# Optimization experiments

Measured on AMD Instinct MI355X. Metric: run time of the kernel, lower is better.

## Reference

```python
import jax, jax.numpy as jnp
import numpy as np

B, S, E = 2, 4096, 768
NH, D = 12, 64
W = 256            # one-sided attention window (attention_window=512 // 2)
NEG = jnp.float32(-1e30)  # stands in for -inf at invalid band positions (safe grads)


def setup_inputs() -> dict:
    key = jax.random.key(0)
    ks = jax.random.split(key, 4)
    sc = 0.02
    return {
        'hidden_states': jax.random.normal(ks[0], (B, S, E), jnp.float32),
        'attention_mask': jnp.zeros((B, S), jnp.float32),   # 0 = local attention everywhere
        'is_index_masked': jnp.zeros((B, S), bool),
        'Wq': jax.random.normal(ks[1], (E, E), jnp.float32) * sc,
        'bq': jnp.zeros((E,), jnp.float32),
        'Wk': jax.random.normal(ks[2], (E, E), jnp.float32) * sc,
        'bk': jnp.zeros((E,), jnp.float32),
        'Wv': jax.random.normal(ks[3], (E, E), jnp.float32) * sc,
        'bv': jnp.zeros((E,), jnp.float32),
    }


def _longformer_local(hidden_states, attention_mask, is_index_masked, Wq, bq, Wk, bk, Wv, bv):
    b, s, e = hidden_states.shape
    w = W
    nc = s // w
    # projections (nn.Linear: x @ W.T + b); query pre-scaled by 1/sqrt(head_dim)
    q = (hidden_states @ Wq.T + bq) / jnp.sqrt(jnp.float32(D))
    k = hidden_states @ Wk.T + bk
    v = hidden_states @ Wv.T + bv
    # [B, NH, S, D]
    q = q.reshape(b, s, NH, D).transpose(0, 2, 1, 3)
    k = k.reshape(b, s, NH, D).transpose(0, 2, 1, 3)
    v = v.reshape(b, s, NH, D).transpose(0, 2, 1, 3)

    # pad keys/values by w on each side; chunk into [B,NH,nc,3w,D] windows
    kp = jnp.pad(k, ((0, 0), (0, 0), (w, w), (0, 0)))
    vp = jnp.pad(v, ((0, 0), (0, 0), (w, w), (0, 0)))
    starts = jnp.arange(nc) * w                      # [nc]
    cidx = starts[:, None] + jnp.arange(3 * w)[None, :]  # [nc, 3w] (padded coords)
    kc = kp[:, :, cidx, :]                            # [B,NH,nc,3w,D]
    vc = vp[:, :, cidx, :]                            # [B,NH,nc,3w,D]
    qc = q.reshape(b, NH, nc, w, D)

    # banded scores: query p in chunk attends keys at offsets p..p+2w within the 3w window
    scores = jnp.einsum('bhcpd,bhckd->bhcpk', qc, kc)  # [B,NH,nc,w,3w]
    p = jnp.arange(w)[:, None]
    koff = jnp.arange(2 * w + 1)[None, :]
    band_idx = p + koff                                # [w, 2w+1]
    band = jnp.take_along_axis(scores, band_idx[None, None, None], axis=-1)  # [B,NH,nc,w,2w+1]

    # additive mask from attention_mask (torch: finfo.min where !=0), gathered at key positions
    fmask = jnp.where(attention_mask != 0, jnp.finfo(jnp.float32).min, jnp.float32(0.0))  # [B,S]
    j = starts[:, None, None] + band_idx[None] - w     # global key index [nc,w,2w+1]
    valid = (j >= 0) & (j < s)
    jc = jnp.clip(j, 0, s - 1)
    band = band + fmask[:, jc][:, None]                # [B,1->NH,nc,w,2w+1]
    # _mask_invalid_locations: out-of-sequence band entries -> -inf (NEG)
    band = jnp.where(valid[None, None], band, NEG)

    probs = jax.nn.softmax(band.astype(jnp.float32), axis=-1)
    # zero probs at fully-masked query positions
    im = is_index_masked.reshape(b, 1, nc, w, 1)
    probs = jnp.where(im, jnp.float32(0.0), probs)

    # scatter band back to [B,NH,nc,w,3w] and contract with value chunks
    full = jnp.zeros((b, NH, nc, w, 3 * w), probs.dtype).at[:, :, :, p, band_idx].set(probs)
    out = jnp.einsum('bhcpk,bhckd->bhcpd', full, vc)   # [B,NH,nc,w,D]
    out = out.reshape(b, NH, s, D).transpose(0, 2, 1, 3).reshape(b, s, e)
    return out


def reference(hidden_states, attention_mask, is_index_masked, Wq, bq, Wk, bk, Wv, bv):
    return _longformer_local(hidden_states, attention_mask, is_index_masked,
                             Wq, bq, Wk, bk, Wv, bv)
```

## Files before the change

kernel.cpp:

```cpp
#include <hip/hip_runtime.h>

typedef __bf16 bf16;
typedef __attribute__((ext_vector_type(8))) __bf16 bf16x8;
typedef __attribute__((ext_vector_type(4))) __bf16 bf16x4;
typedef __attribute__((ext_vector_type(4))) float f32x4;

#define MFMA16(a, b, c) __builtin_amdgcn_mfma_f32_16x16x32_bf16((a), (b), (c), 0, 0, 0)

#define S_LEN 4096
#define NHEAD 12
#define EMB   768
#define NEGV  (-1e30f)

__global__ __launch_bounds__(256) void cvt_kernel(const float* __restrict__ x,
                                                  bf16* __restrict__ o, int n8, float scale) {
  int i = blockIdx.x * 256 + threadIdx.x;
  if (i >= n8) return;
  const float4* p = (const float4*)(x + (size_t)i * 8);
  float4 a = p[0], b = p[1];
  bf16x8 v;
  v[0] = (bf16)(a.x * scale); v[1] = (bf16)(a.y * scale);
  v[2] = (bf16)(a.z * scale); v[3] = (bf16)(a.w * scale);
  v[4] = (bf16)(b.x * scale); v[5] = (bf16)(b.y * scale);
  v[6] = (bf16)(b.z * scale); v[7] = (bf16)(b.w * scale);
  *(bf16x8*)(o + (size_t)i * 8) = v;
}

__global__ __launch_bounds__(256) void qkv_gemm(const bf16* __restrict__ Xb, const bf16* __restrict__ Wb,
                                                const float* __restrict__ bq, const float* __restrict__ bk,
                                                const float* __restrict__ bv,
                                                bf16* __restrict__ Qo, bf16* __restrict__ Ko,
                                                bf16* __restrict__ Vt) {
  __shared__ union SM {
    struct { bf16 a[128 * 64]; bf16 b[128 * 64]; } st;
    bf16 c[128 * 130];
  } sm;
  const int tid = threadIdx.x;
  const int l = tid & 63, w = tid >> 6;
  const int ln = l & 15, g = l >> 4;
  const int wm = w >> 1, wn = w & 1;
  const int m0 = blockIdx.x * 128;
  const int n0 = blockIdx.y * 128;

  const f32x4 zero4 = {0.f, 0.f, 0.f, 0.f};
  f32x4 acc[4][4];
#pragma unroll
  for (int i = 0; i < 4; ++i)
#pragma unroll
    for (int j = 0; j < 4; ++j) acc[i][j] = zero4;

  for (int kt = 0; kt < 12; ++kt) {
    const int k0 = kt * 64;
#pragma unroll
    for (int p = 0; p < 4; ++p) {
      int G = p * 256 + tid;
      int row = G >> 3, slot = G & 7;
      int dsl = slot ^ (row & 7);
      bf16x8 va = *(const bf16x8*)(Xb + (size_t)(m0 + row) * 768 + k0 + slot * 8);
      *(bf16x8*)(&sm.st.a[row * 64 + dsl * 8]) = va;
      bf16x8 vb = *(const bf16x8*)(Wb + (size_t)(n0 + row) * 768 + k0 + slot * 8);
      *(bf16x8*)(&sm.st.b[row * 64 + dsl * 8]) = vb;
    }
    __syncthreads();
#pragma unroll
    for (int kc = 0; kc < 2; ++kc) {
      bf16x8 af[4], bfr[4];
#pragma unroll
      for (int i = 0; i < 4; ++i) {
        int ra = wm * 64 + i * 16 + ln;
        af[i] = *(const bf16x8*)(&sm.st.a[ra * 64 + ((kc * 4 + g) ^ (ra & 7)) * 8]);
        int rb = wn * 64 + i * 16 + ln;
        bfr[i] = *(const bf16x8*)(&sm.st.b[rb * 64 + ((kc * 4 + g) ^ (rb & 7)) * 8]);
      }
#pragma unroll
      for (int mi = 0; mi < 4; ++mi)
#pragma unroll
        for (int ni = 0; ni < 4; ++ni)
          acc[mi][ni] = MFMA16(af[mi], bfr[ni], acc[mi][ni]);
    }
    __syncthreads();
  }

  const int which = n0 / 768;
  const int h0 = (n0 % 768) >> 6;
  const int b = m0 >> 12;
  const int h = h0 + wn;
  const float bsc = (which == 0) ? 0.125f : 1.0f;
  const float* bias = (which == 0) ? bq : (which == 1) ? bk : bv;
  float bvv[4];
#pragma unroll
  for (int ni = 0; ni < 4; ++ni) bvv[ni] = bias[h * 64 + ni * 16 + ln] * bsc;

  if (which < 2) {
    bf16* dst = (which == 0) ? Qo : Ko;
    const size_t base = ((size_t)(b * NHEAD + h) * S_LEN + (m0 & 4095)) * 64;
#pragma unroll
    for (int mi = 0; mi < 4; ++mi)
#pragma unroll
      for (int ni = 0; ni < 4; ++ni)
#pragma unroll
        for (int r = 0; r < 4; ++r) {
          int sl = wm * 64 + mi * 16 + g * 4 + r;
          dst[base + (size_t)sl * 64 + ni * 16 + ln] = (bf16)(acc[mi][ni][r] + bvv[ni]);
        }
  } else {
#pragma unroll
    for (int mi = 0; mi < 4; ++mi)
#pragma unroll
      for (int ni = 0; ni < 4; ++ni)
#pragma unroll
        for (int r = 0; r < 4; ++r) {
          int sl = wm * 64 + mi * 16 + g * 4 + r;
          sm.c[sl * 130 + wn * 64 + ni * 16 + ln] = (bf16)(acc[mi][ni][r] + bvv[ni]);
        }
    __syncthreads();
#pragma unroll
    for (int it = 0; it < 4; ++it) {
      int d = it * 32 + (tid >> 3);
      int scp = tid & 7;
      int hh = h0 + (d >> 6);
      bf16x8 o0, o1;
#pragma unroll
      for (int i2 = 0; i2 < 8; ++i2) o0[i2] = sm.c[(scp * 16 + i2) * 130 + d];
#pragma unroll
      for (int i2 = 0; i2 < 8; ++i2) o1[i2] = sm.c[(scp * 16 + 8 + i2) * 130 + d];
      bf16* dp = Vt + ((size_t)(b * NHEAD + hh) * 64 + (d & 63)) * S_LEN + (m0 & 4095) + scp * 16;
      *(bf16x8*)dp = o0;
      *(bf16x8*)(dp + 8) = o1;
    }
  }
}

__global__ __launch_bounds__(256) void attn_kernel(const bf16* __restrict__ Qb, const bf16* __restrict__ Kb,
                                                   const bf16* __restrict__ Vtb,
                                                   const float* __restrict__ amask,
                                                   const unsigned char* __restrict__ imask,
                                                   float* __restrict__ out) {
  __shared__ bf16 Ks[64 * 64];
  __shared__ bf16 Vs[64 * 64];
  __shared__ bf16 Pt[4][16 * 64];
  __shared__ float Ams[64];
  const int tid = threadIdx.x;
  const int l = tid & 63, w = tid >> 6;
  const int ln = l & 15, g = l >> 4;
  const int bh = blockIdx.y, b = bh / NHEAD, h = bh % NHEAD;
  const int q0 = blockIdx.x * 64;
  const int qg = q0 + w * 16 + ln;

  const size_t qoff = ((size_t)bh * S_LEN + qg) * 64;
  const bf16x8 qf0 = *(const bf16x8*)(Qb + qoff + g * 8);
  const bf16x8 qf1 = *(const bf16x8*)(Qb + qoff + 32 + g * 8);

  const f32x4 zero4 = {0.f, 0.f, 0.f, 0.f};
  f32x4 acc[4];
#pragma unroll
  for (int i = 0; i < 4; ++i) acc[i] = zero4;
  float mrun = -1e38f, lrun = 0.f;

  for (int t = 0; t < 9; ++t) {
    const int tj0 = q0 - 256 + t * 64;
    if (tj0 < 0 || tj0 >= S_LEN) continue;
#pragma unroll
    for (int p = 0; p < 2; ++p) {
      int G = p * 256 + tid;
      int row = G >> 3, slot = G & 7;
      int dsl = slot ^ (row & 7);
      *(bf16x8*)(&Ks[row * 64 + dsl * 8]) =
          *(const bf16x8*)(Kb + ((size_t)bh * S_LEN + tj0 + row) * 64 + slot * 8);
      *(bf16x8*)(&Vs[row * 64 + dsl * 8]) =
          *(const bf16x8*)(Vtb + ((size_t)bh * 64 + row) * S_LEN + tj0 + slot * 8);
    }
    if (tid < 64) Ams[tid] = amask[b * S_LEN + tj0 + tid];
    __syncthreads();

    f32x4 sc[4];
#pragma unroll
    for (int i = 0; i < 4; ++i) sc[i] = zero4;
#pragma unroll
    for (int kc = 0; kc < 2; ++kc) {
      bf16x8 qf = kc ? qf1 : qf0;
#pragma unroll
      for (int mi = 0; mi < 4; ++mi) {
        int r = mi * 16 + ln;
        bf16x8 kf = *(const bf16x8*)(&Ks[r * 64 + ((kc * 4 + g) ^ (r & 7)) * 8]);
        sc[mi] = MFMA16(kf, qf, sc[mi]);
      }
    }

    float mt = -1e38f;
    float pv[4][4];
#pragma unroll
    for (int mi = 0; mi < 4; ++mi)
#pragma unroll
      for (int r = 0; r < 4; ++r) {
        int key = mi * 16 + g * 4 + r;
        int j = tj0 + key;
        float v = sc[mi][r];
        bool valid = (j >= qg - 256) && (j <= qg + 256);
        v = valid ? ((Ams[key] != 0.f) ? NEGV : v) : NEGV;
        sc[mi][r] = v;
        mt = fmaxf(mt, v);
      }
    mt = fmaxf(mt, __shfl_xor(mt, 16));
    mt = fmaxf(mt, __shfl_xor(mt, 32));
    float mnew = fmaxf(mrun, mt);
    float corr = __expf(mrun - mnew);
    float psum = 0.f;
#pragma unroll
    for (int mi = 0; mi < 4; ++mi)
#pragma unroll
      for (int r = 0; r < 4; ++r) {
        float p = __expf(sc[mi][r] - mnew);
        pv[mi][r] = p;
        psum += p;
      }
    psum += __shfl_xor(psum, 16);
    psum += __shfl_xor(psum, 32);
    lrun = lrun * corr + psum;
    mrun = mnew;
#pragma unroll
    for (int i = 0; i < 4; ++i) acc[i] *= corr;

    bf16* PtW = &Pt[w][0];
#pragma unroll
    for (int mi = 0; mi < 4; ++mi) {
      bf16x4 pk;
      pk[0] = (bf16)pv[mi][0]; pk[1] = (bf16)pv[mi][1];
      pk[2] = (bf16)pv[mi][2]; pk[3] = (bf16)pv[mi][3];
      *(bf16x4*)(&PtW[ln * 64 + ((mi * 4 + g) ^ ln) * 4]) = pk;
    }

#pragma unroll
    for (int ds2 = 0; ds2 < 4; ++ds2) {
#pragma unroll
      for (int kc = 0; kc < 2; ++kc) {
        int r = ds2 * 16 + ln;
        bf16x8 vf = *(const bf16x8*)(&Vs[r * 64 + ((kc * 4 + g) ^ (r & 7)) * 8]);
        bf16x4 pa = *(const bf16x4*)(&PtW[ln * 64 + ((kc * 8 + g * 2) ^ ln) * 4]);
        bf16x4 pb = *(const bf16x4*)(&PtW[ln * 64 + ((kc * 8 + g * 2 + 1) ^ ln) * 4]);
        bf16x8 pf = __builtin_shufflevector(pa, pb, 0, 1, 2, 3, 4, 5, 6, 7);
        acc[ds2] = MFMA16(vf, pf, acc[ds2]);
      }
    }
    __syncthreads();
  }

  float rl = 1.0f / lrun;
  if (imask[b * S_LEN + qg] != 0) rl = 0.0f;
  float* ob = out + ((size_t)b * S_LEN + qg) * EMB + h * 64;
#pragma unroll
  for (int ds2 = 0; ds2 < 4; ++ds2) {
    float4 o;
    o.x = acc[ds2][0] * rl; o.y = acc[ds2][1] * rl;
    o.z = acc[ds2][2] * rl; o.w = acc[ds2][3] * rl;
    *(float4*)(ob + ds2 * 16 + g * 4) = o;
  }
}

extern "C" void kernel_launch(void* const* d_in, const int* in_sizes, int n_in,
                              void* d_out, int out_size, void* d_ws, size_t ws_size,
                              hipStream_t stream) {
  const float* X = (const float*)d_in[0];
  const float* amask = (const float*)d_in[1];
  const unsigned char* imask = (const unsigned char*)d_in[2];
  const float* Wq = (const float*)d_in[3];
  const float* bq = (const float*)d_in[4];
  const float* Wk = (const float*)d_in[5];
  const float* bk = (const float*)d_in[6];
  const float* Wv = (const float*)d_in[7];
  const float* bv = (const float*)d_in[8];
  float* out = (float*)d_out;

  bf16* Xb = (bf16*)d_ws;
  bf16* Wb = Xb + 6291456;
  bf16* Qb = Wb + 3 * 589824;
  bf16* Kb = Qb + 6291456;
  bf16* Vt = Kb + 6291456;

  cvt_kernel<<<3072, 256, 0, stream>>>(X, Xb, 6291456 / 8, 1.0f);
  cvt_kernel<<<288, 256, 0, stream>>>(Wq, Wb, 589824 / 8, 0.125f);
  cvt_kernel<<<288, 256, 0, stream>>>(Wk, Wb + 589824, 589824 / 8, 1.0f);
  cvt_kernel<<<288, 256, 0, stream>>>(Wv, Wb + 2 * 589824, 589824 / 8, 1.0f);
  qkv_gemm<<<dim3(64, 18), 256, 0, stream>>>(Xb, Wb, bq, bk, bv, Qb, Kb, Vt);
  attn_kernel<<<dim3(64, 24), 256, 0, stream>>>(Qb, Kb, Vt, amask, imask, out);
}
```

Baseline: 207.4 us.

## Double-buffer attention tiles with direct-to-LDS loads, larger blocks, lazy rescale, fused weight cast

Several changes land together. The attention kernel now works on 128-query blocks with 512 threads and double-buffers K/V tiles in LDS, filled through global_load_lds, so the next tile loads while the current one computes. It also remaps blocks so nearby heads share an XCD, skips key tiles that fall outside the sequence, and takes a mask-free fast path for interior tiles. The running max is only rescaled when it grows by more than a threshold, and MFMA sections get raised priority. The QKV GEMM also uses direct-to-LDS loads, and the three weight conversions are merged into one launch, which adds LDS pressure and some complexity in exchange for lower latency.

```diff
diff --git a/kernel.cpp b/kernel.cpp
--- a/kernel.cpp
+++ b/kernel.cpp
@@ -11,6 +11,11 @@
 #define NHEAD 12
 #define EMB   768
 #define NEGV  (-1e30f)
+
+__device__ __forceinline__ void gload16(const bf16* g, bf16* l) {
+  __builtin_amdgcn_global_load_lds((const __attribute__((address_space(1))) void*)g,
+                                   (__attribute__((address_space(3))) void*)l, 16, 0, 0);
+}
 
 __global__ __launch_bounds__(256) void cvt_kernel(const float* __restrict__ x,
                                                   bf16* __restrict__ o, int n8, float scale) {
@@ -24,6 +29,25 @@
   v[4] = (bf16)(b.x * scale); v[5] = (bf16)(b.y * scale);
   v[6] = (bf16)(b.z * scale); v[7] = (bf16)(b.w * scale);
   *(bf16x8*)(o + (size_t)i * 8) = v;
+}
+
+__global__ __launch_bounds__(256) void cvt3_kernel(const float* __restrict__ w0,
+                                                   const float* __restrict__ w1,
+                                                   const float* __restrict__ w2,
+                                                   bf16* __restrict__ o, int n8) {
+  int which = blockIdx.y;
+  const float* src = (which == 0) ? w0 : (which == 1) ? w1 : w2;
+  float scale = (which == 0) ? 0.125f : 1.0f;
+  int i = blockIdx.x * 256 + threadIdx.x;
+  if (i >= n8) return;
+  const float4* p = (const float4*)(src + (size_t)i * 8);
+  float4 a = p[0], b = p[1];
+  bf16x8 v;
+  v[0] = (bf16)(a.x * scale); v[1] = (bf16)(a.y * scale);
+  v[2] = (bf16)(a.z * scale); v[3] = (bf16)(a.w * scale);
+  v[4] = (bf16)(b.x * scale); v[5] = (bf16)(b.y * scale);
+  v[6] = (bf16)(b.z * scale); v[7] = (bf16)(b.w * scale);
+  *(bf16x8*)(o + ((size_t)which * n8 + i) * 8) = v;
 }
 
 __global__ __launch_bounds__(256) void qkv_gemm(const bf16* __restrict__ Xb, const bf16* __restrict__ Wb,
@@ -52,15 +76,14 @@
   for (int kt = 0; kt < 12; ++kt) {
     const int k0 = kt * 64;
 #pragma unroll
-    for (int p = 0; p < 4; ++p) {
-      int G = p * 256 + tid;
-      int row = G >> 3, slot = G & 7;
-      int dsl = slot ^ (row & 7);
-      bf16x8 va = *(const bf16x8*)(Xb + (size_t)(m0 + row) * 768 + k0 + slot * 8);
-      *(bf16x8*)(&sm.st.a[row * 64 + dsl * 8]) = va;
-      bf16x8 vb = *(const bf16x8*)(Wb + (size_t)(n0 + row) * 768 + k0 + slot * 8);
-      *(bf16x8*)(&sm.st.b[row * 64 + dsl * 8]) = vb;
-    }
+    for (int i = 0; i < 4; ++i) {
+      const int G = w * 256 + i * 64 + l;
+      const int row = G >> 3, dsl = G & 7;
+      const int slot = dsl ^ (row & 7);
+      gload16(Xb + (size_t)(m0 + row) * 768 + k0 + slot * 8, &sm.st.a[(w * 256 + i * 64) * 8]);
+      gload16(Wb + (size_t)(n0 + row) * 768 + k0 + slot * 8, &sm.st.b[(w * 256 + i * 64) * 8]);
+    }
+    asm volatile("s_waitcnt vmcnt(0)" ::: "memory");
     __syncthreads();
 #pragma unroll
     for (int kc = 0; kc < 2; ++kc) {
@@ -131,20 +154,23 @@
   }
 }
 
-__global__ __launch_bounds__(256) void attn_kernel(const bf16* __restrict__ Qb, const bf16* __restrict__ Kb,
+__global__ __launch_bounds__(512) void attn_kernel(const bf16* __restrict__ Qb, const bf16* __restrict__ Kb,
                                                    const bf16* __restrict__ Vtb,
                                                    const float* __restrict__ amask,
                                                    const unsigned char* __restrict__ imask,
                                                    float* __restrict__ out) {
-  __shared__ bf16 Ks[64 * 64];
-  __shared__ bf16 Vs[64 * 64];
-  __shared__ bf16 Pt[4][16 * 64];
-  __shared__ float Ams[64];
+  __shared__ bf16 Ks[2][64 * 64];
+  __shared__ bf16 Vs[2][64 * 64];
+  __shared__ bf16 Pt[8][16 * 64];
+  __shared__ float Ams[2][64];
   const int tid = threadIdx.x;
   const int l = tid & 63, w = tid >> 6;
   const int ln = l & 15, g = l >> 4;
-  const int bh = blockIdx.y, b = bh / NHEAD, h = bh % NHEAD;
-  const int q0 = blockIdx.x * 64;
+  const int orig = blockIdx.x;
+  const int lb = (orig & 7) * 96 + (orig >> 3);
+  const int qc = lb & 31, bh = lb >> 5;
+  const int b = bh / NHEAD, h = bh % NHEAD;
+  const int q0 = qc * 128;
   const int qg = q0 + w * 16 + ln;
 
   const size_t qoff = ((size_t)bh * S_LEN + qg) * 64;
@@ -157,69 +183,96 @@
   for (int i = 0; i < 4; ++i) acc[i] = zero4;
   float mrun = -1e38f, lrun = 0.f;
 
-  for (int t = 0; t < 9; ++t) {
+  const int t_lo = (q0 >= 256) ? 0 : ((256 - q0) >> 6);
+  int t_hi = (S_LEN + 256 - q0) >> 6;
+  if (t_hi > 10) t_hi = 10;
+
+  auto stage = [&](int sb, int t) {
     const int tj0 = q0 - 256 + t * 64;
-    if (tj0 < 0 || tj0 >= S_LEN) continue;
-#pragma unroll
-    for (int p = 0; p < 2; ++p) {
-      int G = p * 256 + tid;
-      int row = G >> 3, slot = G & 7;
-      int dsl = slot ^ (row & 7);
-      *(bf16x8*)(&Ks[row * 64 + dsl * 8]) =
-          *(const bf16x8*)(Kb + ((size_t)bh * S_LEN + tj0 + row) * 64 + slot * 8);
-      *(bf16x8*)(&Vs[row * 64 + dsl * 8]) =
-          *(const bf16x8*)(Vtb + ((size_t)bh * 64 + row) * S_LEN + tj0 + slot * 8);
-    }
-    if (tid < 64) Ams[tid] = amask[b * S_LEN + tj0 + tid];
-    __syncthreads();
+    const int G = w * 64 + l;
+    const int row = G >> 3, dsl = G & 7;
+    const int slot = dsl ^ (row & 7);
+    gload16(Kb + ((size_t)bh * S_LEN + tj0 + row) * 64 + slot * 8, &Ks[sb][w * 512]);
+    gload16(Vtb + ((size_t)bh * 64 + row) * S_LEN + tj0 + slot * 8, &Vs[sb][w * 512]);
+    if (tid < 64) {
+      float am = amask[b * S_LEN + tj0 + tid];
+      Ams[sb][tid] = (am != 0.f) ? -1e30f : 0.f;
+    }
+  };
+
+  stage(0, t_lo);
+  asm volatile("s_waitcnt vmcnt(0)" ::: "memory");
+  __syncthreads();
+
+  int buf = 0;
+  for (int t = t_lo; t < t_hi; ++t, buf ^= 1) {
+    if (t + 1 < t_hi) stage(buf ^ 1, t + 1);
+    const int tj0 = q0 - 256 + t * 64;
 
     f32x4 sc[4];
 #pragma unroll
     for (int i = 0; i < 4; ++i) sc[i] = zero4;
+    __builtin_amdgcn_s_setprio(1);
 #pragma unroll
     for (int kc = 0; kc < 2; ++kc) {
       bf16x8 qf = kc ? qf1 : qf0;
 #pragma unroll
       for (int mi = 0; mi < 4; ++mi) {
         int r = mi * 16 + ln;
-        bf16x8 kf = *(const bf16x8*)(&Ks[r * 64 + ((kc * 4 + g) ^ (r & 7)) * 8]);
+        bf16x8 kf = *(const bf16x8*)(&Ks[buf][r * 64 + ((kc * 4 + g) ^ (r & 7)) * 8]);
         sc[mi] = MFMA16(kf, qf, sc[mi]);
       }
     }
+    __builtin_amdgcn_s_setprio(0);
 
     float mt = -1e38f;
-    float pv[4][4];
-#pragma unroll
-    for (int mi = 0; mi < 4; ++mi)
-#pragma unroll
-      for (int r = 0; r < 4; ++r) {
-        int key = mi * 16 + g * 4 + r;
-        int j = tj0 + key;
-        float v = sc[mi][r];
-        bool valid = (j >= qg - 256) && (j <= qg + 256);
-        v = valid ? ((Ams[key] != 0.f) ? NEGV : v) : NEGV;
-        sc[mi][r] = v;
-        mt = fmaxf(mt, v);
-      }
+    const bool full = (t * 64 >= w * 16 + 15) && (t * 64 <= w * 16 + 449);
+    if (full) {
+#pragma unroll
+      for (int mi = 0; mi < 4; ++mi)
+#pragma unroll
+        for (int r = 0; r < 4; ++r) {
+          int key = mi * 16 + g * 4 + r;
+          float v = sc[mi][r] + Ams[buf][key];
+          sc[mi][r] = v;
+          mt = fmaxf(mt, v);
+        }
+    } else {
+#pragma unroll
+      for (int mi = 0; mi < 4; ++mi)
+#pragma unroll
+        for (int r = 0; r < 4; ++r) {
+          int key = mi * 16 + g * 4 + r;
+          int j = tj0 + key;
+          bool valid = (j >= qg - 256) && (j <= qg + 256);
+          float v = valid ? (sc[mi][r] + Ams[buf][key]) : NEGV;
+          sc[mi][r] = v;
+          mt = fmaxf(mt, v);
+        }
+    }
     mt = fmaxf(mt, __shfl_xor(mt, 16));
     mt = fmaxf(mt, __shfl_xor(mt, 32));
-    float mnew = fmaxf(mrun, mt);
-    float corr = __expf(mrun - mnew);
+    if (!__all(mt <= mrun + 8.f)) {
+      float mnew = fmaxf(mrun, mt);
+      float corr = __expf(mrun - mnew);
+      lrun *= corr;
+#pragma unroll
+      for (int i = 0; i < 4; ++i) acc[i] *= corr;
+      mrun = mnew;
+    }
     float psum = 0.f;
+    float pv[4][4];
 #pragma unroll
     for (int mi = 0; mi < 4; ++mi)
 #pragma unroll
       for (int r = 0; r < 4; ++r) {
-        float p = __expf(sc[mi][r] - mnew);
+        float p = __expf(sc[mi][r] - mrun);
         pv[mi][r] = p;
         psum += p;
       }
     psum += __shfl_xor(psum, 16);
     psum += __shfl_xor(psum, 32);
-    lrun = lrun * corr + psum;
-    mrun = mnew;
-#pragma unroll
-    for (int i = 0; i < 4; ++i) acc[i] *= corr;
+    lrun += psum;
 
     bf16* PtW = &Pt[w][0];
 #pragma unroll
@@ -230,18 +283,22 @@
       *(bf16x4*)(&PtW[ln * 64 + ((mi * 4 + g) ^ ln) * 4]) = pk;
     }
 
+    __builtin_amdgcn_s_setprio(1);
 #pragma unroll
     for (int ds2 = 0; ds2 < 4; ++ds2) {
 #pragma unroll
       for (int kc = 0; kc < 2; ++kc) {
         int r = ds2 * 16 + ln;
-        bf16x8 vf = *(const bf16x8*)(&Vs[r * 64 + ((kc * 4 + g) ^ (r & 7)) * 8]);
+        bf16x8 vf = *(const bf16x8*)(&Vs[buf][r * 64 + ((kc * 4 + g) ^ (r & 7)) * 8]);
         bf16x4 pa = *(const bf16x4*)(&PtW[ln * 64 + ((kc * 8 + g * 2) ^ ln) * 4]);
         bf16x4 pb = *(const bf16x4*)(&PtW[ln * 64 + ((kc * 8 + g * 2 + 1) ^ ln) * 4]);
         bf16x8 pf = __builtin_shufflevector(pa, pb, 0, 1, 2, 3, 4, 5, 6, 7);
         acc[ds2] = MFMA16(vf, pf, acc[ds2]);
       }
     }
+    __builtin_amdgcn_s_setprio(0);
+
+    asm volatile("s_waitcnt vmcnt(0)" ::: "memory");
     __syncthreads();
   }
 
@@ -278,9 +335,7 @@
   bf16* Vt = Kb + 6291456;
 
   cvt_kernel<<<3072, 256, 0, stream>>>(X, Xb, 6291456 / 8, 1.0f);
-  cvt_kernel<<<288, 256, 0, stream>>>(Wq, Wb, 589824 / 8, 0.125f);
-  cvt_kernel<<<288, 256, 0, stream>>>(Wk, Wb + 589824, 589824 / 8, 1.0f);
-  cvt_kernel<<<288, 256, 0, stream>>>(Wv, Wb + 2 * 589824, 589824 / 8, 1.0f);
+  cvt3_kernel<<<dim3(288, 3), 256, 0, stream>>>(Wq, Wk, Wv, Wb, 589824 / 8);
   qkv_gemm<<<dim3(64, 18), 256, 0, stream>>>(Xb, Wb, bq, bk, bv, Qb, Kb, Vt);
-  attn_kernel<<<dim3(64, 24), 256, 0, stream>>>(Qb, Kb, Vt, amask, imask, out);
-}
+  attn_kernel<<<768, 512, 0, stream>>>(Qb, Kb, Vt, amask, imask, out);
+}
```

Result: faster. 186.3 us (-10.2%).
